# Kernel tuning notes

Hardware: AMD Instinct MI355X
Metric: run time of the kernel (lower is better)

The kernel has to match this reference:

```python
import jax, jax.numpy as jnp
import numpy as np

V, E_DIM, H, B, T = 390, 256, 512, 64, 512
START = 388


def setup_inputs() -> dict:
    key = jax.random.key(0)
    ks = jax.random.split(key, 32)
    s = 0.05
    rn = lambda k, shape: jax.random.normal(k, shape, jnp.float32) * s
    inp = {
        "input": jax.random.normal(ks[0], (B, T, V), jnp.float32),
        # encoder params
        "enc_emb": rn(ks[1], (V, E_DIM)),
        "enc_Wih0": rn(ks[2], (3 * H, E_DIM)),
        "enc_Whh0": rn(ks[3], (3 * H, H)),
        "enc_bih0": rn(ks[4], (3 * H,)),
        "enc_bhh0": rn(ks[5], (3 * H,)),
        "enc_Wih1": rn(ks[6], (3 * H, H)),
        "enc_Whh1": rn(ks[7], (3 * H, H)),
        "enc_bih1": rn(ks[8], (3 * H,)),
        "enc_bhh1": rn(ks[9], (3 * H,)),
        # decoder params
        "dec_emb": rn(ks[10], (V, E_DIM)),
        "dec_Wih0": rn(ks[11], (3 * H, E_DIM)),
        "dec_Whh0": rn(ks[12], (3 * H, H)),
        "dec_bih0": rn(ks[13], (3 * H,)),
        "dec_bhh0": rn(ks[14], (3 * H,)),
        "dec_Wih1": rn(ks[15], (3 * H, H)),
        "dec_Whh1": rn(ks[16], (3 * H, H)),
        "dec_bih1": rn(ks[17], (3 * H,)),
        "dec_bhh1": rn(ks[18], (3 * H,)),
        # prediction head
        "Wp1": rn(ks[19], (H, H)),
        "bp1": rn(ks[20], (H,)),
        "Wp2": rn(ks[21], (V, H)),
        "bp2": rn(ks[22], (V,)),
    }
    return inp


def _gru_cell(x, h, Wih, Whh, bih, bhh):
    # PyTorch GRU cell: gates ordered (r, z, n)
    gi = x @ Wih.T + bih
    gh = h @ Whh.T + bhh
    ir, iz, inn = jnp.split(gi, 3, axis=-1)
    hr, hz, hn = jnp.split(gh, 3, axis=-1)
    r = jax.nn.sigmoid(ir + hr)
    z = jax.nn.sigmoid(iz + hz)
    n = jnp.tanh(inn + r * hn)
    return (1.0 - z) * n + z * h


def reference(input, enc_emb, enc_Wih0, enc_Whh0, enc_bih0, enc_bhh0,
              enc_Wih1, enc_Whh1, enc_bih1, enc_bhh1,
              dec_emb, dec_Wih0, dec_Whh0, dec_bih0, dec_bhh0,
              dec_Wih1, dec_Whh1, dec_bih1, dec_bhh1,
              Wp1, bp1, Wp2, bp2):
    batch, max_len, vocab = input.shape
    hdim = enc_Whh0.shape[1]

    # ---- Encoder: soft embedding + 2-layer GRU, keep final hidden states ----
    x = jnp.einsum('btv,ve->bte', input, enc_emb)  # [B,T,E]
    xt = jnp.transpose(x, (1, 0, 2))               # time-major [T,B,E]
    h0 = jnp.zeros((batch, hdim), input.dtype)

    def step0(h, xt_):
        h = _gru_cell(xt_, h, enc_Wih0, enc_Whh0, enc_bih0, enc_bhh0)
        return h, h
    h1_enc, seq1 = jax.lax.scan(step0, h0, xt)

    def step1(h, xt_):
        h = _gru_cell(xt_, h, enc_Wih1, enc_Whh1, enc_bih1, enc_bhh1)
        return h, None
    h2_enc, _ = jax.lax.scan(step1, h0, seq1)

    tok0 = jnp.full((batch,), START, jnp.int32)
    rng0 = jax.random.key(42)

    def dec_step(carry, _):
        h1, h2, tok, rng = carry
        rng, sk = jax.random.split(rng)
        xe = dec_emb[tok]                               # [B,E]
        h1 = _gru_cell(xe, h1, dec_Wih0, dec_Whh0, dec_bih0, dec_bhh0)
        h2 = _gru_cell(h1, h2, dec_Wih1, dec_Whh1, dec_bih1, dec_bhh1)
        hid = h2 @ Wp1.T + bp1
        hid = jnp.where(hid >= 0, hid, 0.1 * hid)       # LeakyReLU(0.1)
        logits = hid @ Wp2.T + bp2                      # temp=1 -> logits/temp == logits
        probs = jax.nn.softmax(logits, axis=-1)
        tok = jax.random.categorical(sk, logits, axis=-1).astype(jnp.int32)
        return (h1, h2, tok, rng), (probs, tok)

    _, (probs_seq, toks) = jax.lax.scan(
        dec_step, (h1_enc, h2_enc, tok0, rng0), None, length=max_len - 1)

    start_oh = jax.nn.one_hot(tok0, vocab, dtype=input.dtype)  # [B,V]
    outputs = jnp.concatenate(
        [start_oh[:, None, :], jnp.transpose(probs_seq, (1, 0, 2))], axis=1)
    max_output = jnp.concatenate(
        [jnp.full((batch, 1), float(START), jnp.float32),
         toks.T.astype(jnp.float32)], axis=1)
    return outputs, max_output
```

## Files before the change

kernel.cpp:

```cpp
#include <hip/hip_runtime.h>
#include <math.h>


#define BB 64
#define TT 512
#define VV 390
#define EE 256
#define HH 512

static __device__ __forceinline__ void tf2x32(unsigned k0, unsigned k1,
                                              unsigned x0, unsigned x1,
                                              unsigned &o0, unsigned &o1) {
  unsigned ks2 = k0 ^ k1 ^ 0x1BD11BDAu;
  x0 += k0; x1 += k1;
#define TFR(r) x0 += x1; x1 = (x1 << (r)) | (x1 >> (32 - (r))); x1 ^= x0;
  TFR(13) TFR(15) TFR(26) TFR(6)
  x0 += k1; x1 += ks2 + 1u;
  TFR(17) TFR(29) TFR(16) TFR(24)
  x0 += ks2; x1 += k0 + 2u;
  TFR(13) TFR(15) TFR(26) TFR(6)
  x0 += k0; x1 += k1 + 3u;
  TFR(17) TFR(29) TFR(16) TFR(24)
  x0 += k1; x1 += ks2 + 4u;
  TFR(13) TFR(15) TFR(26) TFR(6)
  x0 += ks2; x1 += k0 + 5u;
#undef TFR
  o0 = x0; o1 = x1;
}

static __device__ __forceinline__ float sigm(float x) {
  return 1.0f / (1.0f + expf(-x));
}

static __device__ __forceinline__ unsigned ldu_a(const unsigned* p) {
  return __hip_atomic_load((unsigned*)p, __ATOMIC_RELAXED,
                           __HIP_MEMORY_SCOPE_AGENT);
}
static __device__ __forceinline__ void stu_a(unsigned* p, unsigned v) {
  __hip_atomic_store(p, v, __ATOMIC_RELAXED, __HIP_MEMORY_SCOPE_AGENT);
}
static __device__ __forceinline__ float ldf_a(const float* p) {
  return __uint_as_float(ldu_a((const unsigned*)p));
}
static __device__ __forceinline__ void stf_a(float* p, float v) {
  stu_a((unsigned*)p, __float_as_uint(v));
}

template <int K>
static __device__ __forceinline__ void dot3_kb(const float* __restrict__ X, int b,
    const float* __restrict__ w0, const float* __restrict__ w1,
    const float* __restrict__ w2, float &r0, float &r1, float &r2) {
  const float4* q0 = (const float4*)w0;
  const float4* q1 = (const float4*)w1;
  const float4* q2 = (const float4*)w2;
  float s0 = 0.f, s1 = 0.f, s2 = 0.f;
#pragma unroll 4
  for (int k4 = 0; k4 < (K >> 2); ++k4) {
    float4 u0 = q0[k4], u1 = q1[k4], u2 = q2[k4];
    int kb = (k4 << 8) + b;
    float x0 = X[kb], x1 = X[kb + 64], x2 = X[kb + 128], x3 = X[kb + 192];
    s0 = fmaf(x0, u0.x, s0); s0 = fmaf(x1, u0.y, s0); s0 = fmaf(x2, u0.z, s0); s0 = fmaf(x3, u0.w, s0);
    s1 = fmaf(x0, u1.x, s1); s1 = fmaf(x1, u1.y, s1); s1 = fmaf(x2, u1.z, s1); s1 = fmaf(x3, u1.w, s1);
    s2 = fmaf(x0, u2.x, s2); s2 = fmaf(x1, u2.y, s2); s2 = fmaf(x2, u2.z, s2); s2 = fmaf(x3, u2.w, s2);
  }
  r0 = s0; r1 = s1; r2 = s2;
}

template <int K>
static __device__ __forceinline__ void dot3_kb_a(const float* __restrict__ X, int b,
    const float* __restrict__ w0, const float* __restrict__ w1,
    const float* __restrict__ w2, float &r0, float &r1, float &r2) {
  const float4* q0 = (const float4*)w0;
  const float4* q1 = (const float4*)w1;
  const float4* q2 = (const float4*)w2;
  float s0 = 0.f, s1 = 0.f, s2 = 0.f;
#pragma unroll 4
  for (int k4 = 0; k4 < (K >> 2); ++k4) {
    float4 u0 = q0[k4], u1 = q1[k4], u2 = q2[k4];
    int kb = (k4 << 8) + b;
    float x0 = ldf_a(X + kb), x1 = ldf_a(X + kb + 64);
    float x2 = ldf_a(X + kb + 128), x3 = ldf_a(X + kb + 192);
    s0 = fmaf(x0, u0.x, s0); s0 = fmaf(x1, u0.y, s0); s0 = fmaf(x2, u0.z, s0); s0 = fmaf(x3, u0.w, s0);
    s1 = fmaf(x0, u1.x, s1); s1 = fmaf(x1, u1.y, s1); s1 = fmaf(x2, u1.z, s1); s1 = fmaf(x3, u1.w, s1);
    s2 = fmaf(x0, u2.x, s2); s2 = fmaf(x1, u2.y, s2); s2 = fmaf(x2, u2.z, s2); s2 = fmaf(x3, u2.w, s2);
  }
  r0 = s0; r1 = s1; r2 = s2;
}

template <int K>
static __device__ __forceinline__ float dot1_kb_a(const float* __restrict__ X, int b,
    const float* __restrict__ w) {
  const float4* q = (const float4*)w;
  float s = 0.f;
#pragma unroll 4
  for (int k4 = 0; k4 < (K >> 2); ++k4) {
    float4 u = q[k4];
    int kb = (k4 << 8) + b;
    s = fmaf(ldf_a(X + kb), u.x, s);
    s = fmaf(ldf_a(X + kb + 64), u.y, s);
    s = fmaf(ldf_a(X + kb + 128), u.z, s);
    s = fmaf(ldf_a(X + kb + 192), u.w, s);
  }
  return s;
}

template <int K>
static __device__ __forceinline__ void dot3_row(const float* __restrict__ xrow,
    const float* __restrict__ w0, const float* __restrict__ w1,
    const float* __restrict__ w2, float &r0, float &r1, float &r2) {
  const float4* xq = (const float4*)xrow;
  const float4* q0 = (const float4*)w0;
  const float4* q1 = (const float4*)w1;
  const float4* q2 = (const float4*)w2;
  float s0 = 0.f, s1 = 0.f, s2 = 0.f;
#pragma unroll 4
  for (int k4 = 0; k4 < (K >> 2); ++k4) {
    float4 x = xq[k4];
    float4 u0 = q0[k4], u1 = q1[k4], u2 = q2[k4];
    s0 = fmaf(x.x, u0.x, s0); s0 = fmaf(x.y, u0.y, s0); s0 = fmaf(x.z, u0.z, s0); s0 = fmaf(x.w, u0.w, s0);
    s1 = fmaf(x.x, u1.x, s1); s1 = fmaf(x.y, u1.y, s1); s1 = fmaf(x.z, u1.z, s1); s1 = fmaf(x.w, u1.w, s1);
    s2 = fmaf(x.x, u2.x, s2); s2 = fmaf(x.y, u2.y, s2); s2 = fmaf(x.z, u2.z, s2); s2 = fmaf(x.w, u2.w, s2);
  }
  r0 = s0; r1 = s1; r2 = s2;
}

template <int NWG>
static __device__ __forceinline__ void flagbar(unsigned* flags, unsigned* go,
                                               int wg, unsigned epoch) {
  __syncthreads();
  int tid = threadIdx.x;
  if (wg == 0) {
    if (tid == 0) stu_a(flags + 0, epoch);
    while (!__syncthreads_and((int)(ldu_a(flags + (tid & (NWG - 1))) >= epoch))) {}
    if (tid < NWG) stu_a(go + tid, epoch);
  } else {
    if (tid == 0) {
      stu_a(flags + wg, epoch);
      while (ldu_a(go + wg) < epoch) __builtin_amdgcn_s_sleep(1);
    }
    __syncthreads();
  }
}

__global__ __launch_bounds__(256) void k_init(float* out,
    float* h1buf, float* h2buf, int* tok, unsigned* ebase) {
  int wg = blockIdx.x, tid = threadIdx.x;
  for (int i = wg * 256 + tid; i < HH * BB; i += 64 * 256) {
    h1buf[i] = 0.f;
    h2buf[i] = 0.f;
  }
  for (int v = tid; v < VV; v += 256)
    out[(size_t)wg * TT * VV + v] = (v == 388) ? 1.0f : 0.0f;
  if (wg == 0) {
    ebase[tid] = 0u;
    ebase[tid + 256] = 0u;
  }
  if (tid == 0) {
    out[(size_t)BB * TT * VV + (size_t)wg * TT] = 388.0f;
    tok[wg] = 388;
  }
}

__global__ __launch_bounds__(256) void k_xgemm(const float* __restrict__ input,
    const float* __restrict__ emb, float* __restrict__ xT) {
  int t = blockIdx.x, tid = threadIdx.x;
  int s = tid >> 6, b = tid & 63;
  __shared__ float lin[64 * 65];
  float4 acc[16];
#pragma unroll
  for (int i = 0; i < 16; ++i) acc[i] = make_float4(0.f, 0.f, 0.f, 0.f);
  for (int k0 = 0; k0 < VV; k0 += 64) {
    int kmax = min(64, VV - k0);
    __syncthreads();
#pragma unroll
    for (int r = 0; r < 16; ++r) {
      int idx = r * 256 + tid;
      int b2 = idx >> 6, kk = idx & 63;
      if (kk < kmax)
        lin[kk * 65 + b2] = input[((size_t)b2 * TT + t) * VV + k0 + kk];
    }
    __syncthreads();
    for (int kk = 0; kk < kmax; ++kk) {
      float xv = lin[kk * 65 + b];
      const float4* er = (const float4*)(emb + (size_t)(k0 + kk) * EE);
#pragma unroll
      for (int i = 0; i < 16; ++i) {
        float4 w = er[s + 4 * i];
        acc[i].x = fmaf(xv, w.x, acc[i].x);
        acc[i].y = fmaf(xv, w.y, acc[i].y);
        acc[i].z = fmaf(xv, w.z, acc[i].z);
        acc[i].w = fmaf(xv, w.w, acc[i].w);
      }
    }
  }
  float* dst0 = xT + (size_t)t * (EE * 64);
#pragma unroll
  for (int i = 0; i < 16; ++i) {
    int e = (s + 4 * i) * 4;
    float* d = dst0 + e * 64 + b;
    d[0] = acc[i].x; d[64] = acc[i].y; d[128] = acc[i].z; d[192] = acc[i].w;
  }
}

__global__ __launch_bounds__(256) void k_enc_persist(
    const float* __restrict__ xT, float* h1buf, float* h2buf,
    const float* __restrict__ Wih0, const float* __restrict__ Whh0,
    const float* __restrict__ bih0, const float* __restrict__ bhh0,
    const float* __restrict__ Wih1, const float* __restrict__ Whh1,
    const float* __restrict__ bih1, const float* __restrict__ bhh1,
    unsigned* ebase, unsigned* dbase) {
  int wg = blockIdx.x, tid = threadIdx.x;
  int s = tid >> 6, b = tid & 63;
  unsigned* eflags = ebase;
  unsigned* ego = ebase + 256;
  for (int t = 0; t <= TT; ++t) {
    const float* h1_r = h1buf + (t & 1) * (HH * BB);
    float* h1_w = h1buf + ((t + 1) & 1) * (HH * BB);
    if (wg < 128) {
      if (t < TT) {
        int j = wg * 4 + s;
        float ar, az, an, hr, hz, hn;
        dot3_kb<EE>(xT + (size_t)t * (EE * 64), b,
                    Wih0 + (size_t)j * EE, Wih0 + (size_t)(512 + j) * EE,
                    Wih0 + (size_t)(1024 + j) * EE, ar, az, an);
        dot3_kb_a<HH>(h1_r, b,
                      Whh0 + (size_t)j * HH, Whh0 + (size_t)(512 + j) * HH,
                      Whh0 + (size_t)(1024 + j) * HH, hr, hz, hn);
        float r = sigm((ar + bih0[j]) + (hr + bhh0[j]));
        float z = sigm((az + bih0[512 + j]) + (hz + bhh0[512 + j]));
        float n = tanhf((an + bih0[1024 + j]) + r * (hn + bhh0[1024 + j]));
        stf_a(&h1_w[j * 64 + b],
              (1.0f - z) * n + z * ldf_a(&h1_r[j * 64 + b]));
      }
    } else {
      if (t >= 1) {
        int j = (wg - 128) * 4 + s;
        const float* h2_r = h2buf + ((t + 1) & 1) * (HH * BB);
        float* h2_w = h2buf + (t & 1) * (HH * BB);
        float ar, az, an, hr, hz, hn;
        dot3_kb_a<HH>(h1_r, b,
                      Wih1 + (size_t)j * HH, Wih1 + (size_t)(512 + j) * HH,
                      Wih1 + (size_t)(1024 + j) * HH, ar, az, an);
        dot3_kb_a<HH>(h2_r, b,
                      Whh1 + (size_t)j * HH, Whh1 + (size_t)(512 + j) * HH,
                      Whh1 + (size_t)(1024 + j) * HH, hr, hz, hn);
        float r = sigm((ar + bih1[j]) + (hr + bhh1[j]));
        float z = sigm((az + bih1[512 + j]) + (hz + bhh1[512 + j]));
        float n = tanhf((an + bih1[1024 + j]) + r * (hn + bhh1[1024 + j]));
        stf_a(&h2_w[j * 64 + b],
              (1.0f - z) * n + z * ldf_a(&h2_r[j * 64 + b]));
      }
    }
    if (t == 2 && wg == 0) stu_a(dbase + tid, 0u);
    if (t < TT) flagbar<256>(eflags, ego, wg, (unsigned)(t + 1));
  }
}

__global__ __launch_bounds__(256) void k_dec_persist(
    float* h1buf, float* h2buf,
    const float* __restrict__ demb,
    const float* __restrict__ dWih0, const float* __restrict__ dWhh0,
    const float* __restrict__ dbih0, const float* __restrict__ dbhh0,
    const float* __restrict__ dWih1, const float* __restrict__ dWhh1,
    const float* __restrict__ dbih1, const float* __restrict__ dbhh1,
    const float* __restrict__ Wp1, const float* __restrict__ bp1,
    const float* __restrict__ Wp2, const float* __restrict__ bp2,
    float* out, int* tok, unsigned* dbase, float* hid, float* lg) {
  int wg = blockIdx.x, tid = threadIdx.x;
  int s = tid >> 6, b = tid & 63;
  unsigned* dflags = dbase;
  unsigned* dgo = dbase + 128;
  __shared__ float rf[8];
  __shared__ int ri[4];
  unsigned rk0 = 0u, rk1 = 42u;
  unsigned ep = 0u;
  for (int d = 0; d < TT - 1; ++d) {
    {
      const float* h1_r = h1buf + (d & 1) * (HH * BB);
      float* h1_w = h1buf + ((d + 1) & 1) * (HH * BB);
      int j = wg * 4 + s;
      int tk = (int)ldu_a((const unsigned*)&tok[b]);
      float ar, az, an, hr, hz, hn;
      dot3_row<EE>(demb + (size_t)tk * EE,
                   dWih0 + (size_t)j * EE, dWih0 + (size_t)(512 + j) * EE,
                   dWih0 + (size_t)(1024 + j) * EE, ar, az, an);
      dot3_kb_a<HH>(h1_r, b,
                    dWhh0 + (size_t)j * HH, dWhh0 + (size_t)(512 + j) * HH,
                    dWhh0 + (size_t)(1024 + j) * HH, hr, hz, hn);
      float r = sigm((ar + dbih0[j]) + (hr + dbhh0[j]));
      float z = sigm((az + dbih0[512 + j]) + (hz + dbhh0[512 + j]));
      float n = tanhf((an + dbih0[1024 + j]) + r * (hn + dbhh0[1024 + j]));
      stf_a(&h1_w[j * 64 + b],
            (1.0f - z) * n + z * ldf_a(&h1_r[j * 64 + b]));
    }
    flagbar<128>(dflags, dgo, wg, ++ep);
    {
      const float* h1n = h1buf + ((d + 1) & 1) * (HH * BB);
      const float* h2r = h2buf + (d & 1) * (HH * BB);
      float* h2w = h2buf + ((d + 1) & 1) * (HH * BB);
      int j = wg * 4 + s;
      float ar, az, an, hr, hz, hn;
      dot3_kb_a<HH>(h1n, b,
                    dWih1 + (size_t)j * HH, dWih1 + (size_t)(512 + j) * HH,
                    dWih1 + (size_t)(1024 + j) * HH, ar, az, an);
      dot3_kb_a<HH>(h2r, b,
                    dWhh1 + (size_t)j * HH, dWhh1 + (size_t)(512 + j) * HH,
                    dWhh1 + (size_t)(1024 + j) * HH, hr, hz, hn);
      float r = sigm((ar + dbih1[j]) + (hr + dbhh1[j]));
      float z = sigm((az + dbih1[512 + j]) + (hz + dbhh1[512 + j]));
      float n = tanhf((an + dbih1[1024 + j]) + r * (hn + dbhh1[1024 + j]));
      stf_a(&h2w[j * 64 + b],
            (1.0f - z) * n + z * ldf_a(&h2r[j * 64 + b]));
    }
    flagbar<128>(dflags, dgo, wg, ++ep);
    {
      const float* h2n = h2buf + ((d + 1) & 1) * (HH * BB);
      int j = wg * 4 + s;
      float a = dot1_kb_a<HH>(h2n, b, Wp1 + (size_t)j * HH);
      a += bp1[j];
      stf_a(&hid[j * 64 + b], (a >= 0.f) ? a : 0.1f * a);
    }
    flagbar<128>(dflags, dgo, wg, ++ep);
    {
      int c = wg * 4 + s;
      if (c < VV) {
        float a = dot1_kb_a<HH>(hid, b, Wp2 + (size_t)c * HH);
        stf_a(&lg[c * 64 + b], a + bp2[c]);
      }
    }
    flagbar<128>(dflags, dgo, wg, ++ep);
    if (wg < BB) {
      int brow = wg;
      float v0 = (tid < VV) ? ldf_a(lg + (size_t)tid * 64 + brow) : 0.f;
      float v1 = (tid + 256 < VV) ? ldf_a(lg + (size_t)(tid + 256) * 64 + brow) : 0.f;
      float m = -INFINITY;
      if (tid < VV) m = fmaxf(m, v0);
      if (tid + 256 < VV) m = fmaxf(m, v1);
      for (int off = 32; off > 0; off >>= 1) m = fmaxf(m, __shfl_down(m, off, 64));
      if ((tid & 63) == 0) rf[tid >> 6] = m;
      __syncthreads();
      if (tid == 0) rf[4] = fmaxf(fmaxf(rf[0], rf[1]), fmaxf(rf[2], rf[3]));
      __syncthreads();
      m = rf[4];
      unsigned sk0, sk1;
      tf2x32(rk0, rk1, 0u, 1u, sk0, sk1);
      float by = -INFINITY; int bc = 0x7fffffff;
      if (tid < VV) {
        unsigned o0, o1;
        tf2x32(sk0, sk1, 0u, (unsigned)(brow * VV + tid), o0, o1);
        unsigned bits = o0 ^ o1;
        float f = __uint_as_float(0x3f800000u | (bits >> 9)) - 1.0f;
        float u = (f > 0.f) ? f : 1.17549435e-38f;
        float g = (float)(-log(-log((double)u)));
        float y = v0 + g;
        if (y > by || (y == by && tid < bc)) { by = y; bc = tid; }
      }
      if (tid + 256 < VV) {
        int c = tid + 256;
        unsigned o0, o1;
        tf2x32(sk0, sk1, 0u, (unsigned)(brow * VV + c), o0, o1);
        unsigned bits = o0 ^ o1;
        float f = __uint_as_float(0x3f800000u | (bits >> 9)) - 1.0f;
        float u = (f > 0.f) ? f : 1.17549435e-38f;
        float g = (float)(-log(-log((double)u)));
        float y = v1 + g;
        if (y > by || (y == by && c < bc)) { by = y; bc = c; }
      }
      for (int off = 32; off > 0; off >>= 1) {
        float oy = __shfl_down(by, off, 64);
        int oc = __shfl_down(bc, off, 64);
        if (oy > by || (oy == by && oc < bc)) { by = oy; bc = oc; }
      }
      if ((tid & 63) == 0) { rf[tid >> 6] = by; ri[tid >> 6] = bc; }
      __syncthreads();
      if (tid == 0) {
        by = rf[0]; bc = ri[0];
        for (int w2 = 1; w2 < 4; ++w2)
          if (rf[w2] > by || (rf[w2] == by && ri[w2] < bc)) { by = rf[w2]; bc = ri[w2]; }
        stu_a((unsigned*)&tok[brow], (unsigned)bc);
        out[(size_t)BB * TT * VV + (size_t)brow * TT + (d + 1)] = (float)bc;
      }
      __syncthreads();
      float e0 = 0.f, e1 = 0.f, ssum = 0.f;
      if (tid < VV) { e0 = expf(v0 - m); ssum += e0; }
      if (tid + 256 < VV) { e1 = expf(v1 - m); ssum += e1; }
      for (int off = 32; off > 0; off >>= 1) ssum += __shfl_down(ssum, off, 64);
      if ((tid & 63) == 0) rf[tid >> 6] = ssum;
      __syncthreads();
      if (tid == 0) rf[4] = (rf[0] + rf[1]) + (rf[2] + rf[3]);
      __syncthreads();
      float S = rf[4];
      float* orow = out + ((size_t)brow * TT + (d + 1)) * VV;
      if (tid < VV) orow[tid] = e0 / S;
      if (tid + 256 < VV) orow[tid + 256] = e1 / S;
    }
    {
      unsigned n0, n1;
      tf2x32(rk0, rk1, 0u, 0u, n0, n1);
      rk0 = n0; rk1 = n1;
    }
    if (d < TT - 2) flagbar<128>(dflags, dgo, wg, ++ep);
  }
}

extern "C" void kernel_launch(void* const* d_in, const int* in_sizes, int n_in,
                              void* d_out, int out_size, void* d_ws, size_t ws_size,
                              hipStream_t stream) {
  (void)in_sizes; (void)n_in; (void)out_size; (void)ws_size;
  const float* input = (const float*)d_in[0];
  const float* e_emb = (const float*)d_in[1];
  const float* eWih0 = (const float*)d_in[2];
  const float* eWhh0 = (const float*)d_in[3];
  const float* ebih0 = (const float*)d_in[4];
  const float* ebhh0 = (const float*)d_in[5];
  const float* eWih1 = (const float*)d_in[6];
  const float* eWhh1 = (const float*)d_in[7];
  const float* ebih1 = (const float*)d_in[8];
  const float* ebhh1 = (const float*)d_in[9];
  const float* d_emb = (const float*)d_in[10];
  const float* dWih0 = (const float*)d_in[11];
  const float* dWhh0 = (const float*)d_in[12];
  const float* dbih0 = (const float*)d_in[13];
  const float* dbhh0 = (const float*)d_in[14];
  const float* dWih1 = (const float*)d_in[15];
  const float* dWhh1 = (const float*)d_in[16];
  const float* dbih1 = (const float*)d_in[17];
  const float* dbhh1 = (const float*)d_in[18];
  const float* Wp1   = (const float*)d_in[19];
  const float* bp1   = (const float*)d_in[20];
  const float* Wp2   = (const float*)d_in[21];
  const float* bp2   = (const float*)d_in[22];
  float* out = (float*)d_out;

  float* xT = (float*)d_ws;
  float* h1buf = xT + (size_t)TT * EE * 64;
  float* h2buf = h1buf + 2 * HH * BB;
  int* tok = (int*)(h2buf + 2 * HH * BB);
  unsigned* ebase = (unsigned*)(out + ((size_t)1 * TT + 1) * VV);
  unsigned* dbase = (unsigned*)xT;
  float* hid = xT + 4096;
  float* lg  = hid + (size_t)HH * BB;

  k_init<<<64, 256, 0, stream>>>(out, h1buf, h2buf, tok, ebase);
  k_xgemm<<<TT, 256, 0, stream>>>(input, e_emb, xT);
  k_enc_persist<<<256, 256, 0, stream>>>(xT, h1buf, h2buf,
      eWih0, eWhh0, ebih0, ebhh0, eWih1, eWhh1, ebih1, ebhh1, ebase, dbase);
  k_dec_persist<<<128, 256, 0, stream>>>(h1buf, h2buf, d_emb,
      dWih0, dWhh0, dbih0, dbhh0, dWih1, dWhh1, dbih1, dbhh1,
      Wp1, bp1, Wp2, bp2, out, tok, dbase, hid, lg);
}
```

Baseline: 84.24 ms.

## Double GRU workgroups, split dot products across waves, flat barrier, swizzled hidden layout

The encoder now runs 512 workgroups and the decoder 256, each handling two hidden units, with the input-side and recurrent dot products split across wave pairs and combined through shared memory. Hidden states use a swizzled layout so each lane reads contiguous pairs with 64-bit atomic loads. The master/go grid barrier is replaced by an all-to-all flag poll. The decoder drops one barrier per step by computing the output-projection logits locally per batch row from an LDS copy of the hidden vector. Costs include more flag polling traffic, reliance on all workgroups being co-resident (launch_bounds 256,2), and redundant Wp2 reads per batch row.

Measured after the change: 74.88 ms. 11.1% less time.

```diff
diff --git a/kernel.cpp b/kernel.cpp
--- a/kernel.cpp
+++ b/kernel.cpp
@@ -7,6 +7,8 @@
 #define VV 390
 #define EE 256
 #define HH 512
+
+#define SW(k, b) ((((k) >> 2) << 8) + ((b) << 2) + ((k) & 3))
 
 static __device__ __forceinline__ void tf2x32(unsigned k0, unsigned k1,
                                               unsigned x0, unsigned x1,
@@ -45,63 +47,69 @@
 static __device__ __forceinline__ void stf_a(float* p, float v) {
   stu_a((unsigned*)p, __float_as_uint(v));
 }
+static __device__ __forceinline__ float2 ldf2_a(const float* p) {
+  unsigned long long v = __hip_atomic_load((unsigned long long*)p,
+      __ATOMIC_RELAXED, __HIP_MEMORY_SCOPE_AGENT);
+  return make_float2(__uint_as_float((unsigned)v),
+                     __uint_as_float((unsigned)(v >> 32)));
+}
 
 template <int K>
-static __device__ __forceinline__ void dot3_kb(const float* __restrict__ X, int b,
+static __device__ __forceinline__ void dot3s_a(const float* __restrict__ X, int b,
     const float* __restrict__ w0, const float* __restrict__ w1,
     const float* __restrict__ w2, float &r0, float &r1, float &r2) {
   const float4* q0 = (const float4*)w0;
   const float4* q1 = (const float4*)w1;
   const float4* q2 = (const float4*)w2;
+  const float* Xb = X + (b << 2);
   float s0 = 0.f, s1 = 0.f, s2 = 0.f;
-#pragma unroll 4
+#pragma unroll
   for (int k4 = 0; k4 < (K >> 2); ++k4) {
+    float2 xa = ldf2_a(Xb + (k4 << 8));
+    float2 xc = ldf2_a(Xb + (k4 << 8) + 2);
     float4 u0 = q0[k4], u1 = q1[k4], u2 = q2[k4];
-    int kb = (k4 << 8) + b;
-    float x0 = X[kb], x1 = X[kb + 64], x2 = X[kb + 128], x3 = X[kb + 192];
-    s0 = fmaf(x0, u0.x, s0); s0 = fmaf(x1, u0.y, s0); s0 = fmaf(x2, u0.z, s0); s0 = fmaf(x3, u0.w, s0);
-    s1 = fmaf(x0, u1.x, s1); s1 = fmaf(x1, u1.y, s1); s1 = fmaf(x2, u1.z, s1); s1 = fmaf(x3, u1.w, s1);
-    s2 = fmaf(x0, u2.x, s2); s2 = fmaf(x1, u2.y, s2); s2 = fmaf(x2, u2.z, s2); s2 = fmaf(x3, u2.w, s2);
+    s0 = fmaf(xa.x, u0.x, s0); s0 = fmaf(xa.y, u0.y, s0); s0 = fmaf(xc.x, u0.z, s0); s0 = fmaf(xc.y, u0.w, s0);
+    s1 = fmaf(xa.x, u1.x, s1); s1 = fmaf(xa.y, u1.y, s1); s1 = fmaf(xc.x, u1.z, s1); s1 = fmaf(xc.y, u1.w, s1);
+    s2 = fmaf(xa.x, u2.x, s2); s2 = fmaf(xa.y, u2.y, s2); s2 = fmaf(xc.x, u2.z, s2); s2 = fmaf(xc.y, u2.w, s2);
   }
   r0 = s0; r1 = s1; r2 = s2;
 }
 
 template <int K>
-static __device__ __forceinline__ void dot3_kb_a(const float* __restrict__ X, int b,
+static __device__ __forceinline__ float dot1s_a(const float* __restrict__ X, int b,
+    const float* __restrict__ w) {
+  const float4* q = (const float4*)w;
+  const float* Xb = X + (b << 2);
+  float s = 0.f;
+#pragma unroll
+  for (int k4 = 0; k4 < (K >> 2); ++k4) {
+    float2 xa = ldf2_a(Xb + (k4 << 8));
+    float2 xc = ldf2_a(Xb + (k4 << 8) + 2);
+    float4 u = q[k4];
+    s = fmaf(xa.x, u.x, s); s = fmaf(xa.y, u.y, s);
+    s = fmaf(xc.x, u.z, s); s = fmaf(xc.y, u.w, s);
+  }
+  return s;
+}
+
+template <int K>
+static __device__ __forceinline__ void dot3s_p(const float* __restrict__ X, int b,
     const float* __restrict__ w0, const float* __restrict__ w1,
     const float* __restrict__ w2, float &r0, float &r1, float &r2) {
   const float4* q0 = (const float4*)w0;
   const float4* q1 = (const float4*)w1;
   const float4* q2 = (const float4*)w2;
+  const float4* Xp = (const float4*)X;
   float s0 = 0.f, s1 = 0.f, s2 = 0.f;
-#pragma unroll 4
+#pragma unroll
   for (int k4 = 0; k4 < (K >> 2); ++k4) {
+    float4 x = Xp[(k4 << 6) + b];
     float4 u0 = q0[k4], u1 = q1[k4], u2 = q2[k4];
-    int kb = (k4 << 8) + b;
-    float x0 = ldf_a(X + kb), x1 = ldf_a(X + kb + 64);
-    float x2 = ldf_a(X + kb + 128), x3 = ldf_a(X + kb + 192);
-    s0 = fmaf(x0, u0.x, s0); s0 = fmaf(x1, u0.y, s0); s0 = fmaf(x2, u0.z, s0); s0 = fmaf(x3, u0.w, s0);
-    s1 = fmaf(x0, u1.x, s1); s1 = fmaf(x1, u1.y, s1); s1 = fmaf(x2, u1.z, s1); s1 = fmaf(x3, u1.w, s1);
-    s2 = fmaf(x0, u2.x, s2); s2 = fmaf(x1, u2.y, s2); s2 = fmaf(x2, u2.z, s2); s2 = fmaf(x3, u2.w, s2);
+    s0 = fmaf(x.x, u0.x, s0); s0 = fmaf(x.y, u0.y, s0); s0 = fmaf(x.z, u0.z, s0); s0 = fmaf(x.w, u0.w, s0);
+    s1 = fmaf(x.x, u1.x, s1); s1 = fmaf(x.y, u1.y, s1); s1 = fmaf(x.z, u1.z, s1); s1 = fmaf(x.w, u1.w, s1);
+    s2 = fmaf(x.x, u2.x, s2); s2 = fmaf(x.y, u2.y, s2); s2 = fmaf(x.z, u2.z, s2); s2 = fmaf(x.w, u2.w, s2);
   }
   r0 = s0; r1 = s1; r2 = s2;
-}
-
-template <int K>
-static __device__ __forceinline__ float dot1_kb_a(const float* __restrict__ X, int b,
-    const float* __restrict__ w) {
-  const float4* q = (const float4*)w;
-  float s = 0.f;
-#pragma unroll 4
-  for (int k4 = 0; k4 < (K >> 2); ++k4) {
-    float4 u = q[k4];
-    int kb = (k4 << 8) + b;
-    s = fmaf(ldf_a(X + kb), u.x, s);
-    s = fmaf(ldf_a(X + kb + 64), u.y, s);
-    s = fmaf(ldf_a(X + kb + 128), u.z, s);
-    s = fmaf(ldf_a(X + kb + 192), u.w, s);
-  }
-  return s;
 }
 
 template <int K>
@@ -113,7 +121,7 @@
   const float4* q1 = (const float4*)w1;
   const float4* q2 = (const float4*)w2;
   float s0 = 0.f, s1 = 0.f, s2 = 0.f;
-#pragma unroll 4
+#pragma unroll
   for (int k4 = 0; k4 < (K >> 2); ++k4) {
     float4 x = xq[k4];
     float4 u0 = q0[k4], u1 = q1[k4], u2 = q2[k4];
@@ -125,21 +133,20 @@
 }
 
 template <int NWG>
-static __device__ __forceinline__ void flagbar(unsigned* flags, unsigned* go,
-                                               int wg, unsigned epoch) {
+static __device__ __forceinline__ void bar(unsigned* flags, int wg, unsigned ep) {
   __syncthreads();
   int tid = threadIdx.x;
-  if (wg == 0) {
-    if (tid == 0) stu_a(flags + 0, epoch);
-    while (!__syncthreads_and((int)(ldu_a(flags + (tid & (NWG - 1))) >= epoch))) {}
-    if (tid < NWG) stu_a(go + tid, epoch);
-  } else {
-    if (tid == 0) {
-      stu_a(flags + wg, epoch);
-      while (ldu_a(go + wg) < epoch) __builtin_amdgcn_s_sleep(1);
-    }
-    __syncthreads();
-  }
+  if (tid == 0) stu_a(flags + wg, ep);
+  if (tid < 64) {
+    bool ok;
+    do {
+      ok = true;
+#pragma unroll
+      for (int i = 0; i < NWG; i += 64)
+        ok &= (ldu_a(flags + i + tid) >= ep);
+    } while (!__all(ok));
+  }
+  __syncthreads();
 }
 
 __global__ __launch_bounds__(256) void k_init(float* out,
@@ -196,67 +203,84 @@
   float* dst0 = xT + (size_t)t * (EE * 64);
 #pragma unroll
   for (int i = 0; i < 16; ++i) {
-    int e = (s + 4 * i) * 4;
-    float* d = dst0 + e * 64 + b;
-    d[0] = acc[i].x; d[64] = acc[i].y; d[128] = acc[i].z; d[192] = acc[i].w;
-  }
-}
-
-__global__ __launch_bounds__(256) void k_enc_persist(
+    *(float4*)(dst0 + (s + 4 * i) * 256 + 4 * b) = acc[i];
+  }
+}
+
+__global__ __launch_bounds__(256, 2) void k_enc(
     const float* __restrict__ xT, float* h1buf, float* h2buf,
     const float* __restrict__ Wih0, const float* __restrict__ Whh0,
     const float* __restrict__ bih0, const float* __restrict__ bhh0,
     const float* __restrict__ Wih1, const float* __restrict__ Whh1,
     const float* __restrict__ bih1, const float* __restrict__ bhh1,
-    unsigned* ebase, unsigned* dbase) {
+    unsigned* eflags, unsigned* dbase) {
   int wg = blockIdx.x, tid = threadIdx.x;
   int s = tid >> 6, b = tid & 63;
-  unsigned* eflags = ebase;
-  unsigned* ego = ebase + 256;
+  int cs = s & 1, task = s >> 1;
+  bool lay1 = (wg >= 256);
+  int j = (lay1 ? (wg - 256) : wg) * 2 + cs;
+  __shared__ float part[2][3][64];
   for (int t = 0; t <= TT; ++t) {
     const float* h1_r = h1buf + (t & 1) * (HH * BB);
     float* h1_w = h1buf + ((t + 1) & 1) * (HH * BB);
-    if (wg < 128) {
-      if (t < TT) {
-        int j = wg * 4 + s;
-        float ar, az, an, hr, hz, hn;
-        dot3_kb<EE>(xT + (size_t)t * (EE * 64), b,
-                    Wih0 + (size_t)j * EE, Wih0 + (size_t)(512 + j) * EE,
-                    Wih0 + (size_t)(1024 + j) * EE, ar, az, an);
-        dot3_kb_a<HH>(h1_r, b,
+    bool active = lay1 ? (t >= 1) : (t < TT);
+    float ar = 0.f, az = 0.f, an = 0.f;
+    if (active) {
+      if (!lay1) {
+        if (task == 0) {
+          dot3s_p<EE>(xT + (size_t)t * (EE * 64), b,
+                      Wih0 + (size_t)j * EE, Wih0 + (size_t)(512 + j) * EE,
+                      Wih0 + (size_t)(1024 + j) * EE, ar, az, an);
+        } else {
+          float hr, hz, hn;
+          dot3s_a<HH>(h1_r, b,
                       Whh0 + (size_t)j * HH, Whh0 + (size_t)(512 + j) * HH,
                       Whh0 + (size_t)(1024 + j) * HH, hr, hz, hn);
+          part[cs][0][b] = hr; part[cs][1][b] = hz; part[cs][2][b] = hn;
+        }
+      } else {
+        if (task == 0) {
+          dot3s_a<HH>(h1_r, b,
+                      Wih1 + (size_t)j * HH, Wih1 + (size_t)(512 + j) * HH,
+                      Wih1 + (size_t)(1024 + j) * HH, ar, az, an);
+        } else {
+          const float* h2_r = h2buf + ((t + 1) & 1) * (HH * BB);
+          float hr, hz, hn;
+          dot3s_a<HH>(h2_r, b,
+                      Whh1 + (size_t)j * HH, Whh1 + (size_t)(512 + j) * HH,
+                      Whh1 + (size_t)(1024 + j) * HH, hr, hz, hn);
+          part[cs][0][b] = hr; part[cs][1][b] = hz; part[cs][2][b] = hn;
+        }
+      }
+    }
+    __syncthreads();
+    if (active && task == 0) {
+      float hr = part[cs][0][b], hz = part[cs][1][b], hn = part[cs][2][b];
+      if (!lay1) {
         float r = sigm((ar + bih0[j]) + (hr + bhh0[j]));
         float z = sigm((az + bih0[512 + j]) + (hz + bhh0[512 + j]));
         float n = tanhf((an + bih0[1024 + j]) + r * (hn + bhh0[1024 + j]));
-        stf_a(&h1_w[j * 64 + b],
-              (1.0f - z) * n + z * ldf_a(&h1_r[j * 64 + b]));
-      }
-    } else {
-      if (t >= 1) {
-        int j = (wg - 128) * 4 + s;
+        float hp = ldf_a(h1_r + SW(j, b));
+        stf_a(h1_w + SW(j, b), (1.0f - z) * n + z * hp);
+      } else {
         const float* h2_r = h2buf + ((t + 1) & 1) * (HH * BB);
         float* h2_w = h2buf + (t & 1) * (HH * BB);
-        float ar, az, an, hr, hz, hn;
-        dot3_kb_a<HH>(h1_r, b,
-                      Wih1 + (size_t)j * HH, Wih1 + (size_t)(512 + j) * HH,
-                      Wih1 + (size_t)(1024 + j) * HH, ar, az, an);
-        dot3_kb_a<HH>(h2_r, b,
-                      Whh1 + (size_t)j * HH, Whh1 + (size_t)(512 + j) * HH,
-                      Whh1 + (size_t)(1024 + j) * HH, hr, hz, hn);
         float r = sigm((ar + bih1[j]) + (hr + bhh1[j]));
         float z = sigm((az + bih1[512 + j]) + (hz + bhh1[512 + j]));
         float n = tanhf((an + bih1[1024 + j]) + r * (hn + bhh1[1024 + j]));
-        stf_a(&h2_w[j * 64 + b],
-              (1.0f - z) * n + z * ldf_a(&h2_r[j * 64 + b]));
-      }
-    }
-    if (t == 2 && wg == 0) stu_a(dbase + tid, 0u);
-    if (t < TT) flagbar<256>(eflags, ego, wg, (unsigned)(t + 1));
-  }
-}
-
-__global__ __launch_bounds__(256) void k_dec_persist(
+        float hp = ldf_a(h2_r + SW(j, b));
+        stf_a(h2_w + SW(j, b), (1.0f - z) * n + z * hp);
+      }
+    }
+    if (t == 2 && wg == 0 && tid < 64) {
+#pragma unroll
+      for (int i = 0; i < 256; i += 64) stu_a(dbase + i + tid, 0u);
+    }
+    if (t < TT) bar<512>(eflags, wg, (unsigned)(t + 1));
+  }
+}
+
+__global__ __launch_bounds__(256) void k_dec(
     float* h1buf, float* h2buf,
     const float* __restrict__ demb,
     const float* __restrict__ dWih0, const float* __restrict__ dWhh0,
@@ -265,74 +289,111 @@
     const float* __restrict__ dbih1, const float* __restrict__ dbhh1,
     const float* __restrict__ Wp1, const float* __restrict__ bp1,
     const float* __restrict__ Wp2, const float* __restrict__ bp2,
-    float* out, int* tok, unsigned* dbase, float* hid, float* lg) {
+    float* out, int* tok, unsigned* dflags, float* hid) {
   int wg = blockIdx.x, tid = threadIdx.x;
   int s = tid >> 6, b = tid & 63;
-  unsigned* dflags = dbase;
-  unsigned* dgo = dbase + 128;
+  int cs = s & 1, task = s >> 1;
+  int j = wg * 2 + cs;
+  __shared__ float part[2][3][64];
+  __shared__ __align__(16) float lhid[HH];
   __shared__ float rf[8];
   __shared__ int ri[4];
   unsigned rk0 = 0u, rk1 = 42u;
   unsigned ep = 0u;
   for (int d = 0; d < TT - 1; ++d) {
+    const float* h1_r = h1buf + (d & 1) * (HH * BB);
+    float* h1_w = h1buf + ((d + 1) & 1) * (HH * BB);
+    const float* h2_r = h2buf + (d & 1) * (HH * BB);
+    float* h2_w = h2buf + ((d + 1) & 1) * (HH * BB);
     {
-      const float* h1_r = h1buf + (d & 1) * (HH * BB);
-      float* h1_w = h1buf + ((d + 1) & 1) * (HH * BB);
-      int j = wg * 4 + s;
-      int tk = (int)ldu_a((const unsigned*)&tok[b]);
-      float ar, az, an, hr, hz, hn;
-      dot3_row<EE>(demb + (size_t)tk * EE,
-                   dWih0 + (size_t)j * EE, dWih0 + (size_t)(512 + j) * EE,
-                   dWih0 + (size_t)(1024 + j) * EE, ar, az, an);
-      dot3_kb_a<HH>(h1_r, b,
+      float ar = 0.f, az = 0.f, an = 0.f;
+      if (task == 1) {
+        float hr, hz, hn;
+        dot3s_a<HH>(h1_r, b,
                     dWhh0 + (size_t)j * HH, dWhh0 + (size_t)(512 + j) * HH,
                     dWhh0 + (size_t)(1024 + j) * HH, hr, hz, hn);
-      float r = sigm((ar + dbih0[j]) + (hr + dbhh0[j]));
-      float z = sigm((az + dbih0[512 + j]) + (hz + dbhh0[512 + j]));
-      float n = tanhf((an + dbih0[1024 + j]) + r * (hn + dbhh0[1024 + j]));
-      stf_a(&h1_w[j * 64 + b],
-            (1.0f - z) * n + z * ldf_a(&h1_r[j * 64 + b]));
-    }
-    flagbar<128>(dflags, dgo, wg, ++ep);
+        part[cs][0][b] = hr; part[cs][1][b] = hz; part[cs][2][b] = hn;
+      } else {
+        int tk = (int)ldu_a((const unsigned*)tok + b);
+        dot3_row<EE>(demb + (size_t)tk * EE,
+                     dWih0 + (size_t)j * EE, dWih0 + (size_t)(512 + j) * EE,
+                     dWih0 + (size_t)(1024 + j) * EE, ar, az, an);
+      }
+      __syncthreads();
+      if (task == 0) {
+        float hr = part[cs][0][b], hz = part[cs][1][b], hn = part[cs][2][b];
+        float r = sigm((ar + dbih0[j]) + (hr + dbhh0[j]));
+        float z = sigm((az + dbih0[512 + j]) + (hz + dbhh0[512 + j]));
+        float n = tanhf((an + dbih0[1024 + j]) + r * (hn + dbhh0[1024 + j]));
+        float hp = ldf_a(h1_r + SW(j, b));
+        stf_a(h1_w + SW(j, b), (1.0f - z) * n + z * hp);
+      }
+    }
+    bar<256>(dflags, wg, ++ep);
     {
-      const float* h1n = h1buf + ((d + 1) & 1) * (HH * BB);
-      const float* h2r = h2buf + (d & 1) * (HH * BB);
-      float* h2w = h2buf + ((d + 1) & 1) * (HH * BB);
-      int j = wg * 4 + s;
-      float ar, az, an, hr, hz, hn;
-      dot3_kb_a<HH>(h1n, b,
+      float ar = 0.f, az = 0.f, an = 0.f;
+      if (task == 1) {
+        float hr, hz, hn;
+        dot3s_a<HH>(h2_r, b,
+                    dWhh1 + (size_t)j * HH, dWhh1 + (size_t)(512 + j) * HH,
+                    dWhh1 + (size_t)(1024 + j) * HH, hr, hz, hn);
+        part[cs][0][b] = hr; part[cs][1][b] = hz; part[cs][2][b] = hn;
+      } else {
+        dot3s_a<HH>(h1_w, b,
                     dWih1 + (size_t)j * HH, dWih1 + (size_t)(512 + j) * HH,
                     dWih1 + (size_t)(1024 + j) * HH, ar, az, an);
-      dot3_kb_a<HH>(h2r, b,
-                    dWhh1 + (size_t)j * HH, dWhh1 + (size_t)(512 + j) * HH,
-                    dWhh1 + (size_t)(1024 + j) * HH, hr, hz, hn);
-      float r = sigm((ar + dbih1[j]) + (hr + dbhh1[j]));
-      float z = sigm((az + dbih1[512 + j]) + (hz + dbhh1[512 + j]));
-      float n = tanhf((an + dbih1[1024 + j]) + r * (hn + dbhh1[1024 + j]));
-      stf_a(&h2w[j * 64 + b],
-            (1.0f - z) * n + z * ldf_a(&h2r[j * 64 + b]));
-    }
-    flagbar<128>(dflags, dgo, wg, ++ep);
-    {
-      const float* h2n = h2buf + ((d + 1) & 1) * (HH * BB);
-      int j = wg * 4 + s;
-      float a = dot1_kb_a<HH>(h2n, b, Wp1 + (size_t)j * HH);
+      }
+      __syncthreads();
+      if (task == 0) {
+        float hr = part[cs][0][b], hz = part[cs][1][b], hn = part[cs][2][b];
+        float r = sigm((ar + dbih1[j]) + (hr + dbhh1[j]));
+        float z = sigm((az + dbih1[512 + j]) + (hz + dbhh1[512 + j]));
+        float n = tanhf((an + dbih1[1024 + j]) + r * (hn + dbhh1[1024 + j]));
+        float hp = ldf_a(h2_r + SW(j, b));
+        stf_a(h2_w + SW(j, b), (1.0f - z) * n + z * hp);
+      }
+    }
+    bar<256>(dflags, wg, ++ep);
+    if (task == 0) {
+      float a = dot1s_a<HH>(h2_w, b, Wp1 + (size_t)j * HH);
       a += bp1[j];
-      stf_a(&hid[j * 64 + b], (a >= 0.f) ? a : 0.1f * a);
-    }
-    flagbar<128>(dflags, dgo, wg, ++ep);
-    {
-      int c = wg * 4 + s;
-      if (c < VV) {
-        float a = dot1_kb_a<HH>(hid, b, Wp2 + (size_t)c * HH);
-        stf_a(&lg[c * 64 + b], a + bp2[c]);
-      }
-    }
-    flagbar<128>(dflags, dgo, wg, ++ep);
+      stf_a(hid + SW(j, b), (a >= 0.f) ? a : 0.1f * a);
+    }
+    bar<256>(dflags, wg, ++ep);
     if (wg < BB) {
       int brow = wg;
-      float v0 = (tid < VV) ? ldf_a(lg + (size_t)tid * 64 + brow) : 0.f;
-      float v1 = (tid + 256 < VV) ? ldf_a(lg + (size_t)(tid + 256) * 64 + brow) : 0.f;
+      if (tid < 128) {
+        float2 ha = ldf2_a(hid + tid * 256 + brow * 4);
+        float2 hb = ldf2_a(hid + tid * 256 + brow * 4 + 2);
+        lhid[4 * tid] = ha.x; lhid[4 * tid + 1] = ha.y;
+        lhid[4 * tid + 2] = hb.x; lhid[4 * tid + 3] = hb.y;
+      }
+      __syncthreads();
+      float v0 = 0.f, v1 = 0.f;
+      if (tid < VV) {
+        const float4* w = (const float4*)(Wp2 + (size_t)tid * HH);
+        float a = 0.f;
+#pragma unroll 8
+        for (int k4 = 0; k4 < HH / 4; ++k4) {
+          float4 q = w[k4];
+          float4 hv = *(const float4*)&lhid[k4 * 4];
+          a = fmaf(hv.x, q.x, a); a = fmaf(hv.y, q.y, a);
+          a = fmaf(hv.z, q.z, a); a = fmaf(hv.w, q.w, a);
+        }
+        v0 = a + bp2[tid];
+      }
+      if (tid + 256 < VV) {
+        const float4* w = (const float4*)(Wp2 + (size_t)(tid + 256) * HH);
+        float a = 0.f;
+#pragma unroll 8
+        for (int k4 = 0; k4 < HH / 4; ++k4) {
+          float4 q = w[k4];
+          float4 hv = *(const float4*)&lhid[k4 * 4];
+          a = fmaf(hv.x, q.x, a); a = fmaf(hv.y, q.y, a);
+          a = fmaf(hv.z, q.z, a); a = fmaf(hv.w, q.w, a);
+        }
+        v1 = a + bp2[tid + 256];
+      }
       float m = -INFINITY;
       if (tid < VV) m = fmaxf(m, v0);
       if (tid + 256 < VV) m = fmaxf(m, v1);
@@ -377,7 +438,7 @@
         by = rf[0]; bc = ri[0];
         for (int w2 = 1; w2 < 4; ++w2)
           if (rf[w2] > by || (rf[w2] == by && ri[w2] < bc)) { by = rf[w2]; bc = ri[w2]; }
-        stu_a((unsigned*)&tok[brow], (unsigned)bc);
+        stu_a((unsigned*)tok + brow, (unsigned)bc);
         out[(size_t)BB * TT * VV + (size_t)brow * TT + (d + 1)] = (float)bc;
       }
       __syncthreads();
@@ -399,7 +460,7 @@
       tf2x32(rk0, rk1, 0u, 0u, n0, n1);
       rk0 = n0; rk1 = n1;
     }
-    if (d < TT - 2) flagbar<128>(dflags, dgo, wg, ++ep);
+    if (d < TT - 2) bar<256>(dflags, wg, ++ep);
   }
 }
 
@@ -437,15 +498,14 @@
   float* h2buf = h1buf + 2 * HH * BB;
   int* tok = (int*)(h2buf + 2 * HH * BB);
   unsigned* ebase = (unsigned*)(out + ((size_t)1 * TT + 1) * VV);
-  unsigned* dbase = (unsigned*)xT;
+  unsigned* dflags = (unsigned*)xT;
   float* hid = xT + 4096;
-  float* lg  = hid + (size_t)HH * BB;
 
   k_init<<<64, 256, 0, stream>>>(out, h1buf, h2buf, tok, ebase);
   k_xgemm<<<TT, 256, 0, stream>>>(input, e_emb, xT);
-  k_enc_persist<<<256, 256, 0, stream>>>(xT, h1buf, h2buf,
-      eWih0, eWhh0, ebih0, ebhh0, eWih1, eWhh1, ebih1, ebhh1, ebase, dbase);
-  k_dec_persist<<<128, 256, 0, stream>>>(h1buf, h2buf, d_emb,
+  k_enc<<<512, 256, 0, stream>>>(xT, h1buf, h2buf,
+      eWih0, eWhh0, ebih0, ebhh0, eWih1, eWhh1, ebih1, ebhh1, ebase, dflags);
+  k_dec<<<256, 256, 0, stream>>>(h1buf, h2buf, d_emb,
       dWih0, dWhh0, dbih0, dbhh0, dWih1, dWhh1, dbih1, dbhh1,
-      Wp1, bp1, Wp2, bp2, out, tok, dbase, hid, lg);
-}
+      Wp1, bp1, Wp2, bp2, out, tok, dflags, hid);
+}
```
